# Optimization experiments

Hardware: AMD Instinct MI355X
Metric: run time of the kernel (lower is better)

## Reference

```python
import jax, jax.numpy as jnp
import numpy as np

IMPOSSIBLE = -10000.0
TAGSET_SIZE = 64
NUM_TAGS = TAGSET_SIZE + 2  # C = 66
START_IDX = NUM_TAGS - 2
STOP_IDX = NUM_TAGS - 1
B, L, D = 32, 1024, 1024


def setup_inputs() -> dict:
    key = jax.random.key(0)
    k1, k2, k3, k4, k5 = jax.random.split(key, 5)
    features = jax.random.normal(k1, (B, L, D), dtype=jnp.float32)
    ys = jax.random.randint(k2, (B, L), 0, TAGSET_SIZE).astype(jnp.int64)
    masks = jnp.ones((B, L), dtype=jnp.float32)
    fc_w = jax.random.normal(k3, (D, NUM_TAGS), dtype=jnp.float32) / np.sqrt(D)
    fc_b = jax.random.normal(k4, (NUM_TAGS,), dtype=jnp.float32) * 0.01
    transitions = jax.random.normal(k5, (NUM_TAGS, NUM_TAGS), dtype=jnp.float32)
    # transitions TO start and FROM stop are impossible (torch indexing [to, from])
    transitions = transitions.at[START_IDX, :].set(IMPOSSIBLE)
    transitions = transitions.at[:, STOP_IDX].set(IMPOSSIBLE)
    return {"features": features, "ys": ys, "masks": masks,
            "fc_w": fc_w, "fc_b": fc_b, "transitions": transitions}


def _forward_algorithm(feats, masks, transitions):
    """CRF partition function. feats: [B,L,C], masks: [B,L] -> [B]."""
    Bb, Ll, C = feats.shape
    scores0 = jnp.full((Bb, C), IMPOSSIBLE, dtype=feats.dtype).at[:, START_IDX].set(0.0)

    def step(scores, xs):
        emit_t, m_t = xs  # emit_t: [B,C], m_t: [B]
        # score_t[b, j] = logsumexp_i( scores[b,i] + trans[j,i] + emit[b,j] )
        score_t = jax.nn.logsumexp(
            scores[:, None, :] + transitions[None, :, :] + emit_t[:, :, None], axis=-1)
        scores = score_t * m_t[:, None] + scores * (1.0 - m_t[:, None])
        return scores, None

    xs = (jnp.swapaxes(feats, 0, 1), jnp.swapaxes(masks, 0, 1))  # [L,B,C], [L,B]
    scores, _ = jax.lax.scan(step, scores0, xs)
    return jax.nn.logsumexp(scores + transitions[STOP_IDX][None, :], axis=-1)


def _score_sentence(feats, tags, masks, transitions):
    """Score of the gold tag path. feats: [B,L,C], tags: [B,L] -> [B]."""
    Bb, Ll, C = feats.shape
    emit = jnp.take_along_axis(feats, tags[:, :, None], axis=2)[:, :, 0]  # [B,L]
    start = jnp.full((Bb, 1), START_IDX, dtype=tags.dtype)
    tags_ext = jnp.concatenate([start, tags], axis=1)  # [B,L+1]
    trans_sc = transitions[tags_ext[:, 1:], tags_ext[:, :-1]]  # [B,L]
    lengths = masks.sum(1).astype(jnp.int32)  # [B]
    last_tag = tags_ext[jnp.arange(Bb), lengths]  # [B]
    last_score = transitions[STOP_IDX, last_tag]
    return ((trans_sc + emit) * masks).sum(1) + last_score


def reference(features, ys, masks, fc_w, fc_b, transitions):
    feats = jnp.einsum('bld,dc->blc', features, fc_w) + fc_b  # [B,L,C]
    masks_ = masks.astype(feats.dtype)
    forward_score = _forward_algorithm(feats, masks_, transitions)  # [B]
    gold_score = _score_sentence(feats, ys.astype(jnp.int32), masks_, transitions)  # [B]
    return (forward_score, gold_score)
```

## Files before the change

kernel.cpp:

```cpp
#include <hip/hip_runtime.h>
#include <hip/hip_bf16.h>
#include <stdint.h>


#define START_IDX 64
#define STOP_IDX 65
#define LN2F 0.6931471805599453f

typedef __attribute__((ext_vector_type(4))) float f32x4;
typedef __attribute__((ext_vector_type(8))) __bf16 bf16x8;
typedef __attribute__((ext_vector_type(4))) __bf16 bf16x4;

__device__ __forceinline__ void gload_lds16(const void* g, void* l) {
  __builtin_amdgcn_global_load_lds(
      (const __attribute__((address_space(1))) void*)g,
      (__attribute__((address_space(3))) void*)l, 16, 0, 0);
}

template <int CTRL>
__device__ __forceinline__ float dpp_mov(float v) {
  return __int_as_float(
      __builtin_amdgcn_update_dpp(0, __float_as_int(v), CTRL, 0xF, 0xF, true));
}
__device__ __forceinline__ float wave_max64(float v) {
  v = fmaxf(v, dpp_mov<0xB1>(v));
  v = fmaxf(v, dpp_mov<0x4E>(v));
  v = fmaxf(v, dpp_mov<0x141>(v));
  v = fmaxf(v, dpp_mov<0x140>(v));
  v = fmaxf(v, dpp_mov<0x142>(v));
  v = fmaxf(v, dpp_mov<0x143>(v));
  return v;
}
__device__ __forceinline__ float wave_sum64(float v) {
  v += dpp_mov<0xB1>(v);
  v += dpp_mov<0x4E>(v);
  v += dpp_mov<0x141>(v);
  v += dpp_mov<0x140>(v);
  v += dpp_mov<0x142>(v);
  v += dpp_mov<0x143>(v);
  return v;
}

__global__ __launch_bounds__(256) void crf_wcvt(const float* __restrict__ W,
                                                unsigned short* __restrict__ Wbt) {
  __shared__ float tile[64][65];
  const int t = threadIdx.x;
  const int kb = blockIdx.x;
#pragma unroll
  for (int i = 0; i < 16; ++i) {
    const int f = i * 256 + t;
    const int k = f >> 6, n = f & 63;
    tile[k][n] = W[(kb * 64 + k) * 66 + n];
  }
  __syncthreads();
#pragma unroll
  for (int i = 0; i < 16; ++i) {
    const int f = i * 256 + t;
    const int n = f >> 6, k = f & 63;
    union { __bf16 h; unsigned short u; } cv;
    cv.h = (__bf16)tile[k][n];
    Wbt[n * 1024 + kb * 64 + k] = cv.u;
  }
}

__global__ __launch_bounds__(256) void crf_fwd(const float* __restrict__ features,
                                               const unsigned short* __restrict__ Wbt,
                                               const float* __restrict__ bias,
                                               const float* __restrict__ masks,
                                               const float* __restrict__ trans,
                                               float* __restrict__ featsOut,
                                               float* __restrict__ chunkP,
                                               int* __restrict__ chunkExp) {
  __shared__ __align__(16) char smem[32768];
  __shared__ float wmax[2][4];
  const int tid = threadIdx.x;
  const int w = tid >> 6, lane = tid & 63, g = lane >> 4, q = lane & 15;
  const int c = blockIdx.x, b = blockIdx.y;
  const int rb = w & 1, cb = w >> 1;

  const float* Abase = features + ((size_t)b << 20) + ((size_t)c << 15);

  {
    const int arow0 = 8 * w + (lane >> 4);
    const int acolb = ((lane & 15) * 16);
    const int brow0 = 16 * w + (lane >> 3);
    const int bcolb = ((lane & 7) * 16);

    f32x4 acc[2];
    acc[0] = (f32x4){0.f, 0.f, 0.f, 0.f};
    acc[1] = (f32x4){0.f, 0.f, 0.f, 0.f};

#pragma unroll
    for (int j = 0; j < 2; ++j) {
      const int row = arow0 + 4 * j;
      gload_lds16((const char*)(Abase + (size_t)row * 1024) +
                      (acolb ^ ((row & 7) << 4)),
                  smem + (8 * w + 4 * j) * 256);
      const int n = brow0 + 8 * j;
      gload_lds16((const char*)(Wbt + (size_t)n * 1024) +
                      (bcolb ^ ((n & 7) << 4)),
                  smem + 16384 + (16 * w + 8 * j) * 128);
    }

    const int sA = (q & 7) << 4;
    for (int kt = 0; kt < 16; ++kt) {
      const int buf = kt & 1;
      __syncthreads();
      if (kt < 15) {
        const int k0 = (kt + 1) * 64;
#pragma unroll
        for (int j = 0; j < 2; ++j) {
          const int row = arow0 + 4 * j;
          gload_lds16((const char*)(Abase + (size_t)row * 1024 + k0) +
                          (acolb ^ ((row & 7) << 4)),
                      smem + (buf ^ 1) * 8192 + (8 * w + 4 * j) * 256);
          const int n = brow0 + 8 * j;
          gload_lds16((const char*)(Wbt + (size_t)n * 1024 + k0) +
                          (bcolb ^ ((n & 7) << 4)),
                      smem + 16384 + (buf ^ 1) * 8192 + (16 * w + 8 * j) * 128);
        }
      }
      const char* Ab = smem + buf * 8192 + (16 * rb + q) * 256;
      const char* Bb = smem + 16384 + buf * 8192;
#pragma unroll
      for (int kk = 0; kk < 2; ++kk) {
        float4 alo = *(const float4*)(Ab + ((kk * 128 + 32 * g) ^ sA));
        float4 ahi = *(const float4*)(Ab + ((kk * 128 + 32 * g + 16) ^ sA));
        bf16x8 af;
        af[0] = (__bf16)alo.x; af[1] = (__bf16)alo.y;
        af[2] = (__bf16)alo.z; af[3] = (__bf16)alo.w;
        af[4] = (__bf16)ahi.x; af[5] = (__bf16)ahi.y;
        af[6] = (__bf16)ahi.z; af[7] = (__bf16)ahi.w;
#pragma unroll
        for (int nt = 0; nt < 2; ++nt) {
          const int n = q + 16 * (2 * cb + nt);
          bf16x8 bf = *(const bf16x8*)(Bb + n * 128 +
                                       ((kk * 64 + 16 * g) ^ ((n & 7) << 4)));
          acc[nt] = __builtin_amdgcn_mfma_f32_16x16x32_bf16(af, bf, acc[nt], 0, 0, 0);
        }
      }
    }
    const float bb0 = bias[q + 32 * cb], bb1 = bias[q + 32 * cb + 16];
    float (*expE)[64] = (float(*)[64])smem;
#pragma unroll
    for (int r = 0; r < 4; ++r) {
      const int tl = 16 * rb + 4 * g + r;
      float* orow = featsOut + (((size_t)(b << 10) + (c << 5) + tl) << 6) +
                    q + 32 * cb;
      const float v0 = acc[0][r] + bb0, v1 = acc[1][r] + bb1;
      orow[0] = v0; orow[16] = v1;
      expE[tl][q + 32 * cb] = __expf(v0);
      expE[tl][q + 32 * cb + 16] = __expf(v1);
    }
  }

  {
    char* T0 = smem + 16384;
    f32x4 z4 = {0.f, 0.f, 0.f, 0.f};
    *(f32x4*)(T0 + tid * 32) = z4;
    *(f32x4*)(T0 + tid * 32 + 16) = z4;
    const int n = tid >> 2, s = tid & 3;
    const int d = (2 * n) ^ ((n & 7) << 4);
    if ((d >> 5) == s)
      *(unsigned short*)(T0 + n * 128 + d) = (unsigned short)0x3F80;
    if (tid < 4) wmax[0][tid] = 1.0f;
  }

  bf16x8 Ea0, Ea1;
  {
    const int i = 16 * w + q;
    const float* tp0 = trans + i * 66 + 8 * g;
    const float* tp1 = tp0 + 32;
#pragma unroll
    for (int e = 0; e < 8; ++e) {
      Ea0[e] = (__bf16)__expf(tp0[e]);
      Ea1[e] = (__bf16)__expf(tp1[e]);
    }
  }

  float pv[4][4];
#pragma unroll
  for (int nt = 0; nt < 4; ++nt)
#pragma unroll
    for (int r = 0; r < 4; ++r)
      pv[nt][r] = ((16 * w + 4 * g + r) == (q + 16 * nt)) ? 1.f : 0.f;

  const int t0 = (c == 0) ? 1 : (c << 5);
  const int t1 = (c << 5) + 32;
  const float* mb = masks + (b << 10);
  const int tml = t0 + lane;
  const float mkv = mb[tml > 1023 ? 1023 : tml];
  float (*expE)[64] = (float(*)[64])smem;

  int e_acc = 0;
  int cur = 0;
  __syncthreads();

  for (int t = t0; t < t1; ++t) {
    const int tl = t - (c << 5);
    const float4 ee = *(const float4*)&expE[tl][16 * w + 4 * g];
    const float m =
        __int_as_float(__builtin_amdgcn_readlane(__float_as_int(mkv), t - t0));
    if (m != 0.f) {
      const char* Tb = smem + 16384 + cur * 8192;
      f32x4 acc[4];
#pragma unroll
      for (int nt = 0; nt < 4; ++nt) {
        const int n = q + 16 * nt;
        const int sw = (n & 7) << 4;
        bf16x8 B0 = *(const bf16x8*)(Tb + n * 128 + ((16 * g) ^ sw));
        bf16x8 B1 = *(const bf16x8*)(Tb + n * 128 + ((64 + 16 * g) ^ sw));
        f32x4 z = {0.f, 0.f, 0.f, 0.f};
        z = __builtin_amdgcn_mfma_f32_16x16x32_bf16(Ea0, B0, z, 0, 0, 0);
        acc[nt] = __builtin_amdgcn_mfma_f32_16x16x32_bf16(Ea1, B1, z, 0, 0, 0);
      }
      const float4 wm = *(const float4*)wmax[cur];
      const float mx = fmaxf(fmaxf(wm.x, wm.y), fmaxf(wm.z, wm.w));
      const int ex = ((__float_as_int(mx) >> 23) & 0xFF) - 127;
      const float sc = __int_as_float((127 - ex) << 23);
      float ce[4];
      ce[0] = ee.x * sc; ce[1] = ee.y * sc; ce[2] = ee.z * sc; ce[3] = ee.w * sc;
      float nmax[4];
#pragma unroll
      for (int nt = 0; nt < 4; ++nt) {
#pragma unroll
        for (int r = 0; r < 4; ++r) {
          float val = acc[nt][r] * ce[r];
          if (m != 1.f) val = m * val + (1.f - m) * sc * pv[nt][r];
          pv[nt][r] = val;
        }
        nmax[nt] = fmaxf(fmaxf(pv[nt][0], pv[nt][1]),
                         fmaxf(pv[nt][2], pv[nt][3]));
      }
      const int nxt = cur ^ 1;
      char* Tw = smem + 16384 + nxt * 8192;
#pragma unroll
      for (int nt = 0; nt < 4; ++nt) {
        bf16x4 o;
        o[0] = (__bf16)pv[nt][0]; o[1] = (__bf16)pv[nt][1];
        o[2] = (__bf16)pv[nt][2]; o[3] = (__bf16)pv[nt][3];
        const int n = q + 16 * nt;
        *(bf16x4*)(Tw + n * 128 + ((32 * w + 8 * g) ^ ((n & 7) << 4))) = o;
      }
      float lm = wave_max64(fmaxf(fmaxf(nmax[0], nmax[1]),
                                  fmaxf(nmax[2], nmax[3])));
      if (lane == 63) wmax[nxt][w] = lm;
      e_acc += ex;
      __syncthreads();
      cur = nxt;
    }
  }

#pragma unroll
  for (int nt = 0; nt < 4; ++nt)
#pragma unroll
    for (int r = 0; r < 4; ++r)
      chunkP[(((size_t)(b * 32 + c)) << 12) + (size_t)(16 * w + 4 * g + r) * 64 +
             q + 16 * nt] = pv[nt][r];
  if (tid == 0) chunkExp[b * 32 + c] = e_acc;
}

__global__ void crf_fin(const float* __restrict__ feats,
                        const int* __restrict__ ys,
                        const float* __restrict__ masks,
                        const float* __restrict__ trans,
                        const float* __restrict__ chunkP,
                        const int* __restrict__ chunkExp,
                        float* __restrict__ out) {
  __shared__ __align__(16) float vb[64];
  const int lane = threadIdx.x;
  const int b = blockIdx.x >> 1;
  if ((blockIdx.x & 1) == 0) {
    float v = __expf(feats[((size_t)b << 16) + lane]) *
              __expf(trans[lane * 66 + START_IDX]);
    int e_acc = 0;
    for (int cc = 0; cc < 32; ++cc) {
      vb[lane] = v;
      __builtin_amdgcn_wave_barrier();
      const float* Pr = chunkP + (((size_t)(b * 32 + cc)) << 12) + (size_t)lane * 64;
      float q0 = 0.f, q1 = 0.f, q2 = 0.f, q3 = 0.f;
#pragma unroll
      for (int j4 = 0; j4 < 16; ++j4) {
        float4 p = *(const float4*)(Pr + 4 * j4);
        float4 x = ((const float4*)vb)[j4];
        q0 = fmaf(p.x, x.x, q0); q1 = fmaf(p.y, x.y, q1);
        q2 = fmaf(p.z, x.z, q2); q3 = fmaf(p.w, x.w, q3);
      }
      const float qq = (q0 + q1) + (q2 + q3);
      float mx = wave_max64(qq);
      mx = __int_as_float(__builtin_amdgcn_readlane(__float_as_int(mx), 63));
      const int ex = ((__float_as_int(mx) >> 23) & 0xFF) - 127;
      v = qq * __int_as_float((127 - ex) << 23);
      e_acc += ex + chunkExp[b * 32 + cc];
      __builtin_amdgcn_wave_barrier();
    }
    const float sum = wave_sum64(v * __expf(trans[STOP_IDX * 66 + lane]));
    const float s =
        __int_as_float(__builtin_amdgcn_readlane(__float_as_int(sum), 63));
    if (lane == 0) out[b] = __logf(s) + (float)e_acc * LN2F;
  } else {
    const float* fb = feats + ((size_t)b << 16);
    const float* mb = masks + (b << 10);
    const int* yb = ys + (b << 10);
    float s = 0.f, cnt = 0.f;
#pragma unroll
    for (int cc = 0; cc < 16; ++cc) {
      const int t = cc * 64 + lane;
      const float m = mb[t];
      const int y = yb[t];
      const int yp = (t == 0) ? START_IDX : yb[t - 1];
      s += (trans[y * 66 + yp] + fb[t * 64 + y]) * m;
      cnt += m;
    }
    float tot = wave_sum64(s);
    float len = wave_sum64(cnt);
    int totb = __builtin_amdgcn_readlane(__float_as_int(tot), 63);
    int lenb = __builtin_amdgcn_readlane(__float_as_int(len), 63);
    if (lane == 0) {
      const int Lr = (int)__int_as_float(lenb);
      const int last = (Lr == 0) ? START_IDX : yb[Lr - 1];
      out[32 + b] = __int_as_float(totb) + trans[STOP_IDX * 66 + last];
    }
  }
}

extern "C" void kernel_launch(void* const* d_in, const int* in_sizes, int n_in,
                              void* d_out, int out_size, void* d_ws, size_t ws_size,
                              hipStream_t stream) {
  const float* features = (const float*)d_in[0];
  const int* ys         = (const int*)d_in[1];
  const float* masks    = (const float*)d_in[2];
  const float* fc_w     = (const float*)d_in[3];
  const float* fc_b     = (const float*)d_in[4];
  const float* trans    = (const float*)d_in[5];
  float* outp = (float*)d_out;

  char* ws = (char*)d_ws;
  float* feats_ws = (float*)ws;
  unsigned short* Wbt = (unsigned short*)(ws + 8388608);
  float* chunkP = (float*)(ws + 8388608 + 131072);
  int* chunkExp = (int*)(ws + 8388608 + 131072 + 16777216);

  crf_wcvt<<<16, 256, 0, stream>>>(fc_w, Wbt);
  dim3 cg(32, 32);
  crf_fwd<<<cg, 256, 0, stream>>>(features, Wbt, fc_b, masks, trans,
                                  feats_ws, chunkP, chunkExp);
  crf_fin<<<64, 64, 0, stream>>>(feats_ws, ys, masks, trans, chunkP, chunkExp, outp);
}
```

Baseline: 291.8 us.

## Run per-chunk transfer products wave-locally with 32x32 MFMA, dropping block barriers

Each block now computes 64 timesteps of the projection GEMM and splits the chunk scan so each wave owns half the columns of one 32-step transfer product. The state stays in registers and is fed to 32x32x16 MFMA through permlane32 swaps, which removes the LDS round trip and the __syncthreads on every timestep. Renormalisation happens only every other step, from a wave-local max, and the final kernel reconciles the two per-half exponents. This cuts the per-step synchronisation and LDS traffic. In exchange the grid has half as many blocks, and the less frequent rescaling gives the accumulated values less overflow headroom.

Measured after the change: 266.7 us. 8.6% less time.

```diff
diff --git a/kernel.cpp b/kernel.cpp
--- a/kernel.cpp
+++ b/kernel.cpp
@@ -8,13 +8,26 @@
 #define LN2F 0.6931471805599453f
 
 typedef __attribute__((ext_vector_type(4))) float f32x4;
+typedef __attribute__((ext_vector_type(16))) float f32x16;
 typedef __attribute__((ext_vector_type(8))) __bf16 bf16x8;
-typedef __attribute__((ext_vector_type(4))) __bf16 bf16x4;
+typedef __attribute__((ext_vector_type(2))) __bf16 bf16x2;
+typedef __attribute__((ext_vector_type(4))) int i32x4;
 
 __device__ __forceinline__ void gload_lds16(const void* g, void* l) {
   __builtin_amdgcn_global_load_lds(
       (const __attribute__((address_space(1))) void*)g,
       (__attribute__((address_space(3))) void*)l, 16, 0, 0);
+}
+
+__device__ __forceinline__ int pack_bf16(float lo, float hi) {
+  bf16x2 t;
+  t[0] = (__bf16)lo;
+  t[1] = (__bf16)hi;
+  return __builtin_bit_cast(int, t);
+}
+
+__device__ __forceinline__ void pl32_swap(int& x, int& y) {
+  asm("v_permlane32_swap_b32 %0, %1" : "+v"(x), "+v"(y));
 }
 
 template <int CTRL>
@@ -63,43 +76,43 @@
   }
 }
 
-__global__ __launch_bounds__(256) void crf_fwd(const float* __restrict__ features,
-                                               const unsigned short* __restrict__ Wbt,
-                                               const float* __restrict__ bias,
-                                               const float* __restrict__ masks,
-                                               const float* __restrict__ trans,
-                                               float* __restrict__ featsOut,
-                                               float* __restrict__ chunkP,
-                                               int* __restrict__ chunkExp) {
-  __shared__ __align__(16) char smem[32768];
-  __shared__ float wmax[2][4];
+__global__ __launch_bounds__(256, 2) void crf_fwd(const float* __restrict__ features,
+                                                  const unsigned short* __restrict__ Wbt,
+                                                  const float* __restrict__ bias,
+                                                  const float* __restrict__ masks,
+                                                  const float* __restrict__ trans,
+                                                  float* __restrict__ featsOut,
+                                                  float* __restrict__ chunkP,
+                                                  int* __restrict__ chunkExp) {
+  __shared__ __align__(16) char smem[49152];
   const int tid = threadIdx.x;
   const int w = tid >> 6, lane = tid & 63, g = lane >> 4, q = lane & 15;
   const int c = blockIdx.x, b = blockIdx.y;
-  const int rb = w & 1, cb = w >> 1;
-
-  const float* Abase = features + ((size_t)b << 20) + ((size_t)c << 15);
 
   {
-    const int arow0 = 8 * w + (lane >> 4);
-    const int acolb = ((lane & 15) * 16);
+    const float* Abase = features + ((size_t)b << 20) + ((size_t)c << 16);
+    const int arow0 = 16 * w + (lane >> 4);
+    const int acolb = (lane & 15) * 16;
     const int brow0 = 16 * w + (lane >> 3);
-    const int bcolb = ((lane & 7) * 16);
-
-    f32x4 acc[2];
-    acc[0] = (f32x4){0.f, 0.f, 0.f, 0.f};
-    acc[1] = (f32x4){0.f, 0.f, 0.f, 0.f};
-
-#pragma unroll
-    for (int j = 0; j < 2; ++j) {
+    const int bcolb = (lane & 7) * 16;
+
+    f32x4 acc[4];
+#pragma unroll
+    for (int nt = 0; nt < 4; ++nt) acc[nt] = (f32x4){0.f, 0.f, 0.f, 0.f};
+
+#pragma unroll
+    for (int j = 0; j < 4; ++j) {
       const int row = arow0 + 4 * j;
       gload_lds16((const char*)(Abase + (size_t)row * 1024) +
                       (acolb ^ ((row & 7) << 4)),
-                  smem + (8 * w + 4 * j) * 256);
+                  smem + (16 * w + 4 * j) * 256);
+    }
+#pragma unroll
+    for (int j = 0; j < 2; ++j) {
       const int n = brow0 + 8 * j;
       gload_lds16((const char*)(Wbt + (size_t)n * 1024) +
                       (bcolb ^ ((n & 7) << 4)),
-                  smem + 16384 + (16 * w + 8 * j) * 128);
+                  smem + 32768 + (16 * w + 8 * j) * 128);
     }
 
     const int sA = (q & 7) << 4;
@@ -109,19 +122,22 @@
       if (kt < 15) {
         const int k0 = (kt + 1) * 64;
 #pragma unroll
-        for (int j = 0; j < 2; ++j) {
+        for (int j = 0; j < 4; ++j) {
           const int row = arow0 + 4 * j;
           gload_lds16((const char*)(Abase + (size_t)row * 1024 + k0) +
                           (acolb ^ ((row & 7) << 4)),
-                      smem + (buf ^ 1) * 8192 + (8 * w + 4 * j) * 256);
+                      smem + (buf ^ 1) * 16384 + (16 * w + 4 * j) * 256);
+        }
+#pragma unroll
+        for (int j = 0; j < 2; ++j) {
           const int n = brow0 + 8 * j;
           gload_lds16((const char*)(Wbt + (size_t)n * 1024 + k0) +
                           (bcolb ^ ((n & 7) << 4)),
-                      smem + 16384 + (buf ^ 1) * 8192 + (16 * w + 8 * j) * 128);
+                      smem + 32768 + (buf ^ 1) * 8192 + (16 * w + 8 * j) * 128);
         }
       }
-      const char* Ab = smem + buf * 8192 + (16 * rb + q) * 256;
-      const char* Bb = smem + 16384 + buf * 8192;
+      const char* Ab = smem + buf * 16384 + (16 * w + q) * 256;
+      const char* Bb = smem + 32768 + buf * 8192;
 #pragma unroll
       for (int kk = 0; kk < 2; ++kk) {
         float4 alo = *(const float4*)(Ab + ((kk * 128 + 32 * g) ^ sA));
@@ -132,132 +148,157 @@
         af[4] = (__bf16)ahi.x; af[5] = (__bf16)ahi.y;
         af[6] = (__bf16)ahi.z; af[7] = (__bf16)ahi.w;
 #pragma unroll
-        for (int nt = 0; nt < 2; ++nt) {
-          const int n = q + 16 * (2 * cb + nt);
+        for (int nt = 0; nt < 4; ++nt) {
+          const int n = q + 16 * nt;
           bf16x8 bf = *(const bf16x8*)(Bb + n * 128 +
                                        ((kk * 64 + 16 * g) ^ ((n & 7) << 4)));
           acc[nt] = __builtin_amdgcn_mfma_f32_16x16x32_bf16(af, bf, acc[nt], 0, 0, 0);
         }
       }
     }
-    const float bb0 = bias[q + 32 * cb], bb1 = bias[q + 32 * cb + 16];
+    const float bb0 = bias[q + 0], bb1 = bias[q + 16];
+    const float bb2 = bias[q + 32], bb3 = bias[q + 48];
     float (*expE)[64] = (float(*)[64])smem;
 #pragma unroll
     for (int r = 0; r < 4; ++r) {
-      const int tl = 16 * rb + 4 * g + r;
-      float* orow = featsOut + (((size_t)(b << 10) + (c << 5) + tl) << 6) +
-                    q + 32 * cb;
+      const int tl = 16 * w + 4 * g + r;
+      float* orow = featsOut + (((size_t)(b << 10) + (c << 6) + tl) << 6) + q;
       const float v0 = acc[0][r] + bb0, v1 = acc[1][r] + bb1;
-      orow[0] = v0; orow[16] = v1;
-      expE[tl][q + 32 * cb] = __expf(v0);
-      expE[tl][q + 32 * cb + 16] = __expf(v1);
-    }
-  }
-
-  {
-    char* T0 = smem + 16384;
-    f32x4 z4 = {0.f, 0.f, 0.f, 0.f};
-    *(f32x4*)(T0 + tid * 32) = z4;
-    *(f32x4*)(T0 + tid * 32 + 16) = z4;
-    const int n = tid >> 2, s = tid & 3;
-    const int d = (2 * n) ^ ((n & 7) << 4);
-    if ((d >> 5) == s)
-      *(unsigned short*)(T0 + n * 128 + d) = (unsigned short)0x3F80;
-    if (tid < 4) wmax[0][tid] = 1.0f;
-  }
-
-  bf16x8 Ea0, Ea1;
-  {
-    const int i = 16 * w + q;
-    const float* tp0 = trans + i * 66 + 8 * g;
-    const float* tp1 = tp0 + 32;
-#pragma unroll
-    for (int e = 0; e < 8; ++e) {
-      Ea0[e] = (__bf16)__expf(tp0[e]);
-      Ea1[e] = (__bf16)__expf(tp1[e]);
-    }
-  }
-
-  float pv[4][4];
-#pragma unroll
-  for (int nt = 0; nt < 4; ++nt)
-#pragma unroll
-    for (int r = 0; r < 4; ++r)
-      pv[nt][r] = ((16 * w + 4 * g + r) == (q + 16 * nt)) ? 1.f : 0.f;
-
-  const int t0 = (c == 0) ? 1 : (c << 5);
-  const int t1 = (c << 5) + 32;
+      const float v2 = acc[2][r] + bb2, v3 = acc[3][r] + bb3;
+      orow[0] = v0; orow[16] = v1; orow[32] = v2; orow[48] = v3;
+      expE[tl][q + 0]  = __expf(v0);
+      expE[tl][q + 16] = __expf(v1);
+      expE[tl][q + 32] = __expf(v2);
+      expE[tl][q + 48] = __expf(v3);
+    }
+  }
+  __syncthreads();
+
+  const int n32 = lane & 31, H = lane >> 5;
+  const int hc = w >> 1;
+  const int hcol = w & 1;
+  const int cc = 2 * c + hc;
+  const int tbase = cc << 5;
+
+  bf16x8 Ea[2][4];
+#pragma unroll
+  for (int a = 0; a < 2; ++a) {
+    const float* tp = trans + (size_t)(32 * a + n32) * 66 + 8 * H;
+#pragma unroll
+    for (int kc = 0; kc < 4; ++kc)
+#pragma unroll
+      for (int e = 0; e < 8; ++e)
+        Ea[a][kc][e] = (__bf16)__expf(tp[16 * kc + e]);
+  }
+
+  float pv[2][16];
+#pragma unroll
+  for (int a = 0; a < 2; ++a)
+#pragma unroll
+    for (int r = 0; r < 16; ++r) {
+      const int row = 32 * a + (r & 3) + 8 * (r >> 2) + 4 * H;
+      pv[a][r] = (row == 32 * hcol + n32) ? 1.f : 0.f;
+    }
+
   const float* mb = masks + (b << 10);
-  const int tml = t0 + lane;
-  const float mkv = mb[tml > 1023 ? 1023 : tml];
+  int tmi = tbase + n32; if (tmi > 1023) tmi = 1023;
+  const float mkv = mb[tmi];
+
+  f32x16 zz;
+#pragma unroll
+  for (int i = 0; i < 16; ++i) zz[i] = 0.f;
+
+  float wmx = 1.f;
+  int e_acc = 0;
   float (*expE)[64] = (float(*)[64])smem;
-
-  int e_acc = 0;
-  int cur = 0;
-  __syncthreads();
-
-  for (int t = t0; t < t1; ++t) {
-    const int tl = t - (c << 5);
-    const float4 ee = *(const float4*)&expE[tl][16 * w + 4 * g];
+  const int ts0 = (cc == 0) ? 1 : 0;
+
+  for (int ts = ts0; ts < 32; ++ts) {
     const float m =
-        __int_as_float(__builtin_amdgcn_readlane(__float_as_int(mkv), t - t0));
-    if (m != 0.f) {
-      const char* Tb = smem + 16384 + cur * 8192;
-      f32x4 acc[4];
-#pragma unroll
-      for (int nt = 0; nt < 4; ++nt) {
-        const int n = q + 16 * nt;
-        const int sw = (n & 7) << 4;
-        bf16x8 B0 = *(const bf16x8*)(Tb + n * 128 + ((16 * g) ^ sw));
-        bf16x8 B1 = *(const bf16x8*)(Tb + n * 128 + ((64 + 16 * g) ^ sw));
-        f32x4 z = {0.f, 0.f, 0.f, 0.f};
-        z = __builtin_amdgcn_mfma_f32_16x16x32_bf16(Ea0, B0, z, 0, 0, 0);
-        acc[nt] = __builtin_amdgcn_mfma_f32_16x16x32_bf16(Ea1, B1, z, 0, 0, 0);
+        __int_as_float(__builtin_amdgcn_readlane(__float_as_int(mkv), ts));
+    if (m == 0.f) continue;
+    const int tl = (hc << 5) + ts;
+
+    int ex = 0; float sc = 1.f;
+    if ((ts & 1) == 0) {
+      const int mxb = __builtin_amdgcn_readlane(__float_as_int(wmx), 63);
+      ex = ((mxb >> 23) & 0xFF) - 127;
+      sc = __int_as_float((127 - ex) << 23);
+    }
+
+    f32x4 ce[2][4];
+#pragma unroll
+    for (int a = 0; a < 2; ++a)
+#pragma unroll
+      for (int u = 0; u < 4; ++u)
+        ce[a][u] = *(const f32x4*)&expE[tl][32 * a + 8 * u + 4 * H];
+
+    int pk0[8], pk1[8];
+#pragma unroll
+    for (int mi = 0; mi < 8; ++mi) {
+      pk0[mi] = pack_bf16(pv[0][2 * mi], pv[0][2 * mi + 1]);
+      pk1[mi] = pack_bf16(pv[1][2 * mi], pv[1][2 * mi + 1]);
+    }
+
+    f32x16 a0, a1;
+#pragma unroll
+    for (int kc = 0; kc < 4; ++kc) {
+      int* pks = (kc >> 1) ? pk1 : pk0;
+      const int bs = 4 * (kc & 1);
+      int x0 = pks[bs + 0], y0 = pks[bs + 2];
+      int x1 = pks[bs + 1], y1 = pks[bs + 3];
+      pl32_swap(x0, y0);
+      pl32_swap(x1, y1);
+      i32x4 bi = {x0, x1, y0, y1};
+      bf16x8 B = __builtin_bit_cast(bf16x8, bi);
+      if (kc == 0) {
+        a0 = __builtin_amdgcn_mfma_f32_32x32x16_bf16(Ea[0][0], B, zz, 0, 0, 0);
+        a1 = __builtin_amdgcn_mfma_f32_32x32x16_bf16(Ea[1][0], B, zz, 0, 0, 0);
+      } else {
+        a0 = __builtin_amdgcn_mfma_f32_32x32x16_bf16(Ea[0][kc], B, a0, 0, 0, 0);
+        a1 = __builtin_amdgcn_mfma_f32_32x32x16_bf16(Ea[1][kc], B, a1, 0, 0, 0);
       }
-      const float4 wm = *(const float4*)wmax[cur];
-      const float mx = fmaxf(fmaxf(wm.x, wm.y), fmaxf(wm.z, wm.w));
-      const int ex = ((__float_as_int(mx) >> 23) & 0xFF) - 127;
-      const float sc = __int_as_float((127 - ex) << 23);
-      float ce[4];
-      ce[0] = ee.x * sc; ce[1] = ee.y * sc; ce[2] = ee.z * sc; ce[3] = ee.w * sc;
-      float nmax[4];
-#pragma unroll
-      for (int nt = 0; nt < 4; ++nt) {
-#pragma unroll
-        for (int r = 0; r < 4; ++r) {
-          float val = acc[nt][r] * ce[r];
-          if (m != 1.f) val = m * val + (1.f - m) * sc * pv[nt][r];
-          pv[nt][r] = val;
-        }
-        nmax[nt] = fmaxf(fmaxf(pv[nt][0], pv[nt][1]),
-                         fmaxf(pv[nt][2], pv[nt][3]));
-      }
-      const int nxt = cur ^ 1;
-      char* Tw = smem + 16384 + nxt * 8192;
-#pragma unroll
-      for (int nt = 0; nt < 4; ++nt) {
-        bf16x4 o;
-        o[0] = (__bf16)pv[nt][0]; o[1] = (__bf16)pv[nt][1];
-        o[2] = (__bf16)pv[nt][2]; o[3] = (__bf16)pv[nt][3];
-        const int n = q + 16 * nt;
-        *(bf16x4*)(Tw + n * 128 + ((32 * w + 8 * g) ^ ((n & 7) << 4))) = o;
-      }
-      float lm = wave_max64(fmaxf(fmaxf(nmax[0], nmax[1]),
-                                  fmaxf(nmax[2], nmax[3])));
-      if (lane == 63) wmax[nxt][w] = lm;
-      e_acc += ex;
-      __syncthreads();
-      cur = nxt;
-    }
-  }
-
-#pragma unroll
-  for (int nt = 0; nt < 4; ++nt)
-#pragma unroll
-    for (int r = 0; r < 4; ++r)
-      chunkP[(((size_t)(b * 32 + c)) << 12) + (size_t)(16 * w + 4 * g + r) * 64 +
-             q + 16 * nt] = pv[nt][r];
-  if (tid == 0) chunkExp[b * 32 + c] = e_acc;
+    }
+
+    float nmx = 0.f;
+    if (m == 1.f) {
+#pragma unroll
+      for (int u = 0; u < 4; ++u)
+#pragma unroll
+        for (int vv = 0; vv < 4; ++vv) {
+          const int r = 4 * u + vv;
+          const float v0 = a0[r] * ce[0][u][vv] * sc;
+          const float v1 = a1[r] * ce[1][u][vv] * sc;
+          pv[0][r] = v0; pv[1][r] = v1;
+          nmx = fmaxf(nmx, fmaxf(v0, v1));
+        }
+    } else {
+#pragma unroll
+      for (int u = 0; u < 4; ++u)
+#pragma unroll
+        for (int vv = 0; vv < 4; ++vv) {
+          const int r = 4 * u + vv;
+          float v0 = a0[r] * ce[0][u][vv] * sc;
+          float v1 = a1[r] * ce[1][u][vv] * sc;
+          v0 = m * v0 + (1.f - m) * sc * pv[0][r];
+          v1 = m * v1 + (1.f - m) * sc * pv[1][r];
+          pv[0][r] = v0; pv[1][r] = v1;
+          nmx = fmaxf(nmx, fmaxf(v0, v1));
+        }
+    }
+    if (ts & 1) wmx = wave_max64(nmx);
+    e_acc += ex;
+  }
+
+  float* Pb = chunkP + (((size_t)(b * 32 + cc)) << 12) + 32 * hcol;
+#pragma unroll
+  for (int a = 0; a < 2; ++a)
+#pragma unroll
+    for (int r = 0; r < 16; ++r) {
+      const int row = 32 * a + (r & 3) + 8 * (r >> 2) + 4 * H;
+      Pb[(size_t)row * 64 + n32] = pv[a][r];
+    }
+  if (lane == 0) chunkExp[((b * 32 + cc) << 1) + hcol] = e_acc;
 }
 
 __global__ void crf_fin(const float* __restrict__ feats,
@@ -275,7 +316,12 @@
               __expf(trans[lane * 66 + START_IDX]);
     int e_acc = 0;
     for (int cc = 0; cc < 32; ++cc) {
-      vb[lane] = v;
+      const int E0 = chunkExp[((b * 32 + cc) << 1)];
+      const int E1 = chunkExp[((b * 32 + cc) << 1) + 1];
+      const int Em = (E0 > E1) ? E0 : E1;
+      int sh = 127 + ((lane < 32) ? E0 : E1) - Em;
+      if (sh < 1) sh = 1;
+      vb[lane] = v * __int_as_float(sh << 23);
       __builtin_amdgcn_wave_barrier();
       const float* Pr = chunkP + (((size_t)(b * 32 + cc)) << 12) + (size_t)lane * 64;
       float q0 = 0.f, q1 = 0.f, q2 = 0.f, q3 = 0.f;
@@ -291,7 +337,7 @@
       mx = __int_as_float(__builtin_amdgcn_readlane(__float_as_int(mx), 63));
       const int ex = ((__float_as_int(mx) >> 23) & 0xFF) - 127;
       v = qq * __int_as_float((127 - ex) << 23);
-      e_acc += ex + chunkExp[b * 32 + cc];
+      e_acc += ex + Em;
       __builtin_amdgcn_wave_barrier();
     }
     const float sum = wave_sum64(v * __expf(trans[STOP_IDX * 66 + lane]));
@@ -342,7 +388,7 @@
   int* chunkExp = (int*)(ws + 8388608 + 131072 + 16777216);
 
   crf_wcvt<<<16, 256, 0, stream>>>(fc_w, Wbt);
-  dim3 cg(32, 32);
+  dim3 cg(16, 32);
   crf_fwd<<<cg, 256, 0, stream>>>(features, Wbt, fc_b, masks, trans,
                                   feats_ws, chunkP, chunkExp);
   crf_fin<<<64, 64, 0, stream>>>(feats_ws, ys, masks, trans, chunkP, chunkExp, outp);
```
